# Performance work log

Measured on AMD Instinct MI355X. Metric: run time of the kernel, lower is better.

The kernel has to match this reference:

```python
import jax, jax.numpy as jnp
import numpy as np

B, N, C = 8, 1024, 768
H = 12
HD = C // H
RANK = 8
SCALE = HD ** -0.5


def setup_inputs() -> dict:
    key = jax.random.key(0)
    ks = jax.random.split(key, 12)
    s = C ** -0.5
    inp = {
        'x': jax.random.normal(ks[0], (B, N, C), jnp.float32),
        'w_qkv': jax.random.normal(ks[1], (3 * C, C), jnp.float32) * s,
        'b_qkv': jax.random.normal(ks[2], (3 * C,), jnp.float32) * 0.02,
        'w_proj': jax.random.normal(ks[3], (C, C), jnp.float32) * s,
        'b_proj': jax.random.normal(ks[4], (C,), jnp.float32) * 0.02,
        # LoRA A matrices (kaiming-uniform-ish); B matrices are zero at init,
        # but use small nonzero values so the adapter path is exercised.
        'q_a': jax.random.normal(ks[5], (RANK, C), jnp.float32) * s,
        'q_b': jax.random.normal(ks[6], (C, RANK), jnp.float32) * 0.01,
        'k_a': jax.random.normal(ks[7], (RANK, C), jnp.float32) * s,
        'k_b': jax.random.normal(ks[8], (C, RANK), jnp.float32) * 0.01,
        'v_a': jax.random.normal(ks[9], (RANK, C), jnp.float32) * s,
        'v_b': jax.random.normal(ks[10], (C, RANK), jnp.float32) * 0.01,
        'o_a': jax.random.normal(ks[11], (RANK, C), jnp.float32) * s,
        'o_b': jax.random.normal(jax.random.fold_in(key, 99), (C, RANK), jnp.float32) * 0.01,
    }
    return inp


def _lora(x, wa, wb):
    # x:[B,N,C], wa:[r,C], wb:[C,r] -> [B,N,C]
    return jnp.einsum('bnr,cr->bnc', jnp.einsum('bnc,rc->bnr', x, wa), wb)


def reference(x, w_qkv, b_qkv, w_proj, b_proj, q_a, q_b, k_a, k_b, v_a, v_b, o_a, o_b):
    # QKV projection + fused LoRA slice-adds
    qkv = jnp.einsum('bnc,dc->bnd', x, w_qkv) + b_qkv  # [B,N,3C]
    q = qkv[:, :, :C] + _lora(x, q_a, q_b)
    k = qkv[:, :, C:2 * C] + _lora(x, k_a, k_b)
    v = qkv[:, :, 2 * C:] + _lora(x, v_a, v_b)
    # [B,H,N,HD]
    q = q.reshape(B, N, H, HD).transpose(0, 2, 1, 3)
    k = k.reshape(B, N, H, HD).transpose(0, 2, 1, 3)
    v = v.reshape(B, N, H, HD).transpose(0, 2, 1, 3)
    attn = jnp.einsum('bhqd,bhkd->bhqk', q, k) * SCALE
    attn = jax.nn.softmax(attn, axis=-1)  # dropout is identity in eval
    o = jnp.einsum('bhqk,bhkd->bhqd', attn, v)
    o = o.transpose(0, 2, 1, 3).reshape(B, N, C)
    out = jnp.einsum('bnc,dc->bnd', o, w_proj) + b_proj + _lora(o, o_a, o_b)
    return out
```

## Files before the change

### kernel.cpp

```cpp
#include <hip/hip_runtime.h>

typedef __attribute__((ext_vector_type(8))) short short8;
typedef __attribute__((ext_vector_type(4))) float f32x4;
typedef __attribute__((ext_vector_type(4))) unsigned short u16x4;
typedef __attribute__((ext_vector_type(4))) unsigned int u32x4;

#define MFMA16(a,b,c) __builtin_amdgcn_mfma_f32_16x16x32_bf16((a),(b),(c),0,0,0)

#define QSCALE 0.1803368801f

__device__ __forceinline__ unsigned short f2bf(float f) {
  unsigned int x = __float_as_uint(f);
  x += 0x7fffu + ((x >> 16) & 1u);
  return (unsigned short)(x >> 16);
}
__device__ __forceinline__ unsigned int cvtpk(float a, float b) {
  unsigned int r;
  asm("v_cvt_pk_bf16_f32 %0, %1, %2" : "=v"(r) : "v"(a), "v"(b));
  return r;
}


__global__ __launch_bounds__(256) void prep(
    const float* __restrict__ x,
    const float* __restrict__ w_qkv,
    const float* __restrict__ w_proj,
    const float* __restrict__ q_a, const float* __restrict__ q_b,
    const float* __restrict__ k_a, const float* __restrict__ k_b,
    const float* __restrict__ v_a, const float* __restrict__ v_b,
    const float* __restrict__ o_a, const float* __restrict__ o_b,
    unsigned short* __restrict__ xf,
    unsigned short* __restrict__ wqkv_eff,
    unsigned short* __restrict__ wproj_eff)
{
  int bid = blockIdx.x;
  if (bid < 6144) {
    int i4 = (bid * 256 + threadIdx.x) * 4;
    int m  = i4 / 768;
    int k4 = i4 - m * 768;
    f32x4 v = *(const f32x4*)&x[i4];
    u16x4 o;
    o.x = f2bf(v.x); o.y = f2bf(v.y); o.z = f2bf(v.z); o.w = f2bf(v.w);
    int kb = k4 >> 5, qd = (k4 >> 3) & 3, j0 = k4 & 7;
    size_t idx = ((size_t)(kb * 512 + (m >> 4)) << 9) +
                 (((qd << 4) + (m & 15)) << 3) + j0;
    *(u16x4*)&xf[idx] = o;
    return;
  }
  const int QKV = 2304 * 768;
  int idx = (bid - 6144) * 256 + threadIdx.x;
  if (idx < QKV) {
    int n = idx / 768, c = idx - n * 768;
    int sec = n / 768;
    int nr = n - sec * 768;
    const float* a; const float* b;
    if (sec == 0)      { a = q_a; b = q_b; }
    else if (sec == 1) { a = k_a; b = k_b; }
    else               { a = v_a; b = v_b; }
    float acc = w_qkv[idx];
    #pragma unroll
    for (int r = 0; r < 8; r++)
      acc += b[nr * 8 + r] * a[r * 768 + c];
    wqkv_eff[idx] = f2bf(acc);
  } else {
    int i2 = idx - QKV;
    int n = i2 / 768, c = i2 - n * 768;
    float acc = w_proj[i2];
    #pragma unroll
    for (int r = 0; r < 8; r++)
      acc += o_b[n * 8 + r] * o_a[r * 768 + c];
    wproj_eff[i2] = f2bf(acc);
  }
}

__global__ __launch_bounds__(256) void gemm_bt(
    const unsigned short* __restrict__ Af,
    const unsigned short* __restrict__ W,
    const float* __restrict__ bias,
    unsigned short* __restrict__ out0,
    unsigned short* __restrict__ out1,
    unsigned short* __restrict__ out2,
    float* __restrict__ outf,
    int K, int Ncols, int mode)
{
  __shared__ alignas(16) unsigned short Ws[64][72];
  const int tid  = threadIdx.x;
  const int wave = tid >> 6;
  const int lane = tid & 63;
  const int quad = lane >> 4;
  const int l16  = lane & 15;
  const int m0 = blockIdx.x * 128;
  const int n0 = blockIdx.y * 64;
  const int M16b = (m0 >> 4) + wave * 2;

  int wr[2], wc[2];
  #pragma unroll
  for (int i = 0; i < 2; i++) { int f = tid + i * 256; wr[i] = f >> 3; wc[i] = (f & 7) << 3; }

  f32x4 wreg[2];
  #pragma unroll
  for (int i = 0; i < 2; i++)
    wreg[i] = *(const f32x4*)&W[(size_t)(n0 + wr[i]) * K + wc[i]];

  short8 aCur[2][2], aNxt[2][2] = {};
  #pragma unroll
  for (int t = 0; t < 2; t++)
    #pragma unroll
    for (int ks = 0; ks < 2; ks++)
      aCur[t][ks] = *(const short8*)&Af[((size_t)(ks * 512 + M16b + t) << 9) + (lane << 3)];

  f32x4 acc[2][4] = {};

  for (int k0 = 0; k0 < K; k0 += 64) {
    __syncthreads();
    #pragma unroll
    for (int i = 0; i < 2; i++) *(f32x4*)&Ws[wr[i]][wc[i]] = wreg[i];
    __syncthreads();
    if (k0 + 64 < K) {
      #pragma unroll
      for (int i = 0; i < 2; i++)
        wreg[i] = *(const f32x4*)&W[(size_t)(n0 + wr[i]) * K + k0 + 64 + wc[i]];
      const int kbn = (k0 + 64) >> 5;
      #pragma unroll
      for (int t = 0; t < 2; t++)
        #pragma unroll
        for (int ks = 0; ks < 2; ks++)
          aNxt[t][ks] = *(const short8*)&Af[((size_t)((kbn + ks) * 512 + M16b + t) << 9) + (lane << 3)];
    }
    #pragma unroll
    for (int ks = 0; ks < 2; ks++) {
      const int kk = ks * 32 + quad * 8;
      short8 b0 = *(const short8*)&Ws[l16][kk];
      short8 b1 = *(const short8*)&Ws[16 + l16][kk];
      short8 b2 = *(const short8*)&Ws[32 + l16][kk];
      short8 b3 = *(const short8*)&Ws[48 + l16][kk];
      acc[0][0] = MFMA16(aCur[0][ks], b0, acc[0][0]);
      acc[0][1] = MFMA16(aCur[0][ks], b1, acc[0][1]);
      acc[0][2] = MFMA16(aCur[0][ks], b2, acc[0][2]);
      acc[0][3] = MFMA16(aCur[0][ks], b3, acc[0][3]);
      acc[1][0] = MFMA16(aCur[1][ks], b0, acc[1][0]);
      acc[1][1] = MFMA16(aCur[1][ks], b1, acc[1][1]);
      acc[1][2] = MFMA16(aCur[1][ks], b2, acc[1][2]);
      acc[1][3] = MFMA16(aCur[1][ks], b3, acc[1][3]);
    }
    #pragma unroll
    for (int t = 0; t < 2; t++)
      #pragma unroll
      for (int ks = 0; ks < 2; ks++)
        aCur[t][ks] = aNxt[t][ks];
  }

  float bv[4];
  #pragma unroll
  for (int j = 0; j < 4; j++) bv[j] = bias[n0 + j * 16 + l16];

  if (mode == 0) {
    const int sec = n0 / 768;
    const int h   = (n0 % 768) >> 6;
    unsigned short* dst = (sec == 0) ? out0 : ((sec == 1) ? out1 : out2);
    const float scl = (sec == 0) ? QSCALE : 1.0f;
    #pragma unroll
    for (int rg = 0; rg < 2; rg++) {
      #pragma unroll
      for (int r = 0; r < 4; r++) {
        int m  = m0 + wave * 32 + rg * 16 + quad * 4 + r;
        int b  = m >> 10, np = m & 1023;
        int bh = b * 12 + h;
        int s = (np & 35) | ((np & 12) << 1) | ((np & 16) >> 2);
        #pragma unroll
        for (int j = 0; j < 4; j++) {
          int d = j * 16 + l16;
          float v = (acc[rg][j][r] + bv[j]) * scl;
          if (sec == 0) {
            dst[((size_t)bh << 16) + ((size_t)np << 6) + d] = f2bf(v);
          } else if (sec == 1) {
            size_t kidx = ((size_t)((np >> 4) * 2 + (d >> 5)) << 9) +
                          ((((d >> 3) & 3) * 16 + (np & 15)) << 3) + (d & 7);
            dst[((size_t)bh << 16) + kidx] = f2bf(v);
          } else {
            size_t vidx = ((size_t)(((np >> 6) * 2 + (s >> 5)) * 4 + (d >> 4)) << 9) +
                          ((((s >> 3) & 3) * 16 + (d & 15)) << 3) + (s & 7);
            dst[((size_t)bh << 16) + vidx] = f2bf(v);
          }
        }
      }
    }
  } else {
    #pragma unroll
    for (int rg = 0; rg < 2; rg++) {
      #pragma unroll
      for (int r = 0; r < 4; r++) {
        int m = m0 + wave * 32 + rg * 16 + quad * 4 + r;
        #pragma unroll
        for (int j = 0; j < 4; j++)
          outf[(size_t)m * Ncols + n0 + j * 16 + l16] = acc[rg][j][r] + bv[j];
      }
    }
  }
}

__global__ __launch_bounds__(256) void attn(
    const unsigned short* __restrict__ q,
    const unsigned short* __restrict__ k,
    const unsigned short* __restrict__ vt,
    unsigned short* __restrict__ of)
{
  const int tid  = threadIdx.x;
  const int wave = tid >> 6;
  const int lane = tid & 63;
  const int quad = lane >> 4;
  const int l16  = lane & 15;
  const int bh = blockIdx.x;
  const int q0 = blockIdx.y * 64;
  const unsigned short* qb = q  + ((size_t)bh << 16);
  const unsigned short* kb = k  + ((size_t)bh << 16);
  const unsigned short* vb = vt + ((size_t)bh << 16);

  short8 bq[2];
  #pragma unroll
  for (int ks = 0; ks < 2; ks++)
    bq[ks] = *(const short8*)&qb[((size_t)(q0 + wave * 16 + l16) << 6) +
                                 ks * 32 + quad * 8];

  union { u32x4 w; short8 h; } onesu;
  onesu.w.x = 0x3F803F80u; onesu.w.y = 0x3F803F80u;
  onesu.w.z = 0x3F803F80u; onesu.w.w = 0x3F803F80u;
  const short8 onesb = onesu.h;

  f32x4 Oacc[4] = {};
  f32x4 lacc = {};

  union PAW { u32x4 w; short8 h; };

  for (int kt = 0; kt < 16; kt++) {
    f32x4 s[4] = {};
    #pragma unroll
    for (int ks = 0; ks < 2; ks++) {
      const unsigned short* gk = kb + ((size_t)((kt * 8 + ks)) << 9) + (lane << 3);
      short8 a0 = *(const short8*)&gk[0];
      short8 a1 = *(const short8*)&gk[1024];
      short8 a2 = *(const short8*)&gk[2048];
      short8 a3 = *(const short8*)&gk[3072];
      s[0] = MFMA16(a0, bq[ks], s[0]);
      s[1] = MFMA16(a1, bq[ks], s[1]);
      s[2] = MFMA16(a2, bq[ks], s[2]);
      s[3] = MFMA16(a3, bq[ks], s[3]);
    }

    f32x4 e[4];
    #pragma unroll
    for (int i = 0; i < 4; i++) {
      e[i].x = exp2f(s[i].x);
      e[i].y = exp2f(s[i].y);
      e[i].z = exp2f(s[i].z);
      e[i].w = exp2f(s[i].w);
    }
    short8 pa[2];
    #pragma unroll
    for (int ks = 0; ks < 2; ks++) {
      PAW pw;
      pw.w.x = cvtpk(e[2 * ks].x,     e[2 * ks].y);
      pw.w.y = cvtpk(e[2 * ks].z,     e[2 * ks].w);
      pw.w.z = cvtpk(e[2 * ks + 1].x, e[2 * ks + 1].y);
      pw.w.w = cvtpk(e[2 * ks + 1].z, e[2 * ks + 1].w);
      pa[ks] = pw.h;
    }

    #pragma unroll
    for (int ks = 0; ks < 2; ks++) {
      const unsigned short* gv = vb + ((size_t)((kt * 2 + ks) * 4) << 9) + (lane << 3);
      short8 v0 = *(const short8*)&gv[0];
      short8 v1 = *(const short8*)&gv[512];
      short8 v2 = *(const short8*)&gv[1024];
      short8 v3 = *(const short8*)&gv[1536];
      Oacc[0] = MFMA16(pa[ks], v0, Oacc[0]);
      Oacc[1] = MFMA16(pa[ks], v1, Oacc[1]);
      Oacc[2] = MFMA16(pa[ks], v2, Oacc[2]);
      Oacc[3] = MFMA16(pa[ks], v3, Oacc[3]);
      lacc    = MFMA16(pa[ks], onesb, lacc);
    }
  }

  const int b = bh / 12, h = bh - (bh / 12) * 12;
  #pragma unroll
  for (int r = 0; r < 4; r++) {
    float inv = 1.0f / lacc[r];
    int np  = q0 + wave * 16 + quad * 4 + r;
    int M16 = b * 64 + (np >> 4);
    int l16m = np & 15;
    #pragma unroll
    for (int j = 0; j < 4; j++) {
      int col = h * 64 + j * 16 + l16;
      int kb2 = col >> 5;
      int qc  = (col >> 3) & 3;
      size_t idx = ((size_t)(kb2 * 512 + M16) << 9) +
                   ((qc * 16 + l16m) << 3) + (l16 & 7);
      of[idx] = f2bf(Oacc[j][r] * inv);
    }
  }
}

extern "C" void kernel_launch(void* const* d_in, const int* in_sizes, int n_in,
                              void* d_out, int out_size, void* d_ws, size_t ws_size,
                              hipStream_t stream) {
  const float* x      = (const float*)d_in[0];
  const float* w_qkv  = (const float*)d_in[1];
  const float* b_qkv  = (const float*)d_in[2];
  const float* w_proj = (const float*)d_in[3];
  const float* b_proj = (const float*)d_in[4];
  const float* q_a    = (const float*)d_in[5];
  const float* q_b    = (const float*)d_in[6];
  const float* k_a    = (const float*)d_in[7];
  const float* k_b    = (const float*)d_in[8];
  const float* v_a    = (const float*)d_in[9];
  const float* v_b    = (const float*)d_in[10];
  const float* o_a    = (const float*)d_in[11];
  const float* o_b    = (const float*)d_in[12];

  char* ws = (char*)d_ws;
  unsigned short* wqkv_eff  = (unsigned short*)(ws + 0);
  unsigned short* wproj_eff = (unsigned short*)(ws + 3538944);
  unsigned short* xf        = (unsigned short*)(ws + 4718592);
  unsigned short* qd        = (unsigned short*)(ws + 17301504);
  unsigned short* kd        = (unsigned short*)(ws + 29884416);
  unsigned short* vtd       = (unsigned short*)(ws + 42467328);
  unsigned short* of        = xf;

  prep<<<dim3(6144 + 9216), dim3(256), 0, stream>>>(
      x, w_qkv, w_proj, q_a, q_b, k_a, k_b, v_a, v_b, o_a, o_b,
      xf, wqkv_eff, wproj_eff);

  gemm_bt<<<dim3(64, 36), dim3(256), 0, stream>>>(
      xf, wqkv_eff, b_qkv, qd, kd, vtd, nullptr, 768, 2304, 0);

  attn<<<dim3(96, 16), dim3(256), 0, stream>>>(qd, kd, vtd, of);

  gemm_bt<<<dim3(64, 12), dim3(256), 0, stream>>>(
      of, wproj_eff, b_proj, nullptr, nullptr, nullptr, (float*)d_out, 768, 768, 1);
}
```

Measured before the change: 217.0 us.

## Stage K/V tiles through double-buffered LDS via global_load_lds in attention

The attention kernel now loads each 64-key K and V tile into shared memory once per block, using asynchronous global-to-LDS loads. Previously each of the four waves fetched the same tiles from global memory on its own. The buffers are double-buffered so the next tile is prefetched while the current one is consumed, with one barrier per iteration. This cuts redundant global/L2 traffic and hides load latency. The cost is extra LDS use and synchronisation, and correctness depends on the compiler waiting for the async LDS writes before the barrier.

```diff
diff --git a/kernel.cpp b/kernel.cpp
--- a/kernel.cpp
+++ b/kernel.cpp
@@ -13,6 +13,11 @@
   unsigned int x = __float_as_uint(f);
   x += 0x7fffu + ((x >> 16) & 1u);
   return (unsigned short)(x >> 16);
+}
+__device__ __forceinline__ void gload16(const unsigned short* g, unsigned short* l) {
+  __builtin_amdgcn_global_load_lds(
+      (const __attribute__((address_space(1))) unsigned int*)g,
+      (__attribute__((address_space(3))) unsigned int*)l, 16, 0, 0);
 }
 __device__ __forceinline__ unsigned int cvtpk(float a, float b) {
   unsigned int r;
@@ -205,6 +210,8 @@
     const unsigned short* __restrict__ vt,
     unsigned short* __restrict__ of)
 {
+  __shared__ alignas(16) unsigned short Ks2[2][4096];
+  __shared__ alignas(16) unsigned short Vs2[2][4096];
   const int tid  = threadIdx.x;
   const int wave = tid >> 6;
   const int lane = tid & 63;
@@ -216,6 +223,12 @@
   const unsigned short* kb = k  + ((size_t)bh << 16);
   const unsigned short* vb = vt + ((size_t)bh << 16);
 
+  const int t8 = tid * 8;
+  gload16(kb + t8,        &Ks2[0][t8]);
+  gload16(kb + 2048 + t8, &Ks2[0][2048 + t8]);
+  gload16(vb + t8,        &Vs2[0][t8]);
+  gload16(vb + 2048 + t8, &Vs2[0][2048 + t8]);
+
   short8 bq[2];
   #pragma unroll
   for (int ks = 0; ks < 2; ks++)
@@ -233,14 +246,25 @@
   union PAW { u32x4 w; short8 h; };
 
   for (int kt = 0; kt < 16; kt++) {
+    const int p = kt & 1;
+    __syncthreads();
+    if (kt < 15) {
+      const unsigned short* gkn = kb + (kt + 1) * 4096 + t8;
+      const unsigned short* gvn = vb + (kt + 1) * 4096 + t8;
+      gload16(gkn,        &Ks2[1 - p][t8]);
+      gload16(gkn + 2048, &Ks2[1 - p][2048 + t8]);
+      gload16(gvn,        &Vs2[1 - p][t8]);
+      gload16(gvn + 2048, &Vs2[1 - p][2048 + t8]);
+    }
+
     f32x4 s[4] = {};
     #pragma unroll
     for (int ks = 0; ks < 2; ks++) {
-      const unsigned short* gk = kb + ((size_t)((kt * 8 + ks)) << 9) + (lane << 3);
-      short8 a0 = *(const short8*)&gk[0];
-      short8 a1 = *(const short8*)&gk[1024];
-      short8 a2 = *(const short8*)&gk[2048];
-      short8 a3 = *(const short8*)&gk[3072];
+      const unsigned short* lk = &Ks2[p][ks * 512 + lane * 8];
+      short8 a0 = *(const short8*)&lk[0];
+      short8 a1 = *(const short8*)&lk[1024];
+      short8 a2 = *(const short8*)&lk[2048];
+      short8 a3 = *(const short8*)&lk[3072];
       s[0] = MFMA16(a0, bq[ks], s[0]);
       s[1] = MFMA16(a1, bq[ks], s[1]);
       s[2] = MFMA16(a2, bq[ks], s[2]);
@@ -268,11 +292,11 @@
 
     #pragma unroll
     for (int ks = 0; ks < 2; ks++) {
-      const unsigned short* gv = vb + ((size_t)((kt * 2 + ks) * 4) << 9) + (lane << 3);
-      short8 v0 = *(const short8*)&gv[0];
-      short8 v1 = *(const short8*)&gv[512];
-      short8 v2 = *(const short8*)&gv[1024];
-      short8 v3 = *(const short8*)&gv[1536];
+      const unsigned short* lv = &Vs2[p][ks * 2048 + lane * 8];
+      short8 v0 = *(const short8*)&lv[0];
+      short8 v1 = *(const short8*)&lv[512];
+      short8 v2 = *(const short8*)&lv[1024];
+      short8 v3 = *(const short8*)&lv[1536];
       Oacc[0] = MFMA16(pa[ks], v0, Oacc[0]);
       Oacc[1] = MFMA16(pa[ks], v1, Oacc[1]);
       Oacc[2] = MFMA16(pa[ks], v2, Oacc[2]);
```

Result: no change. 215.8 us (-0.6%).
